# Kernel tuning notes

Measured on AMD Instinct MI355X. Metric: run time of the kernel, lower is better.

## Reference

```python
import jax, jax.numpy as jnp
import numpy as np

ALPHA, BETA, THETA = 1.0, 1.0, 10.0
WIN_SIZE = 11
SIGMA = 1.5


def _gauss_window(size, sigma, channel):
    g = np.exp(-((np.arange(size) - size // 2) ** 2) / (2.0 * sigma ** 2))
    g = g / g.sum()
    w2 = np.outer(g, g).astype(np.float32)  # [k, k]
    return jnp.asarray(np.tile(w2[None, None], (channel, 1, 1, 1)))  # [C,1,k,k]


def _dwconv_valid(x, w):
    # x: [B,C,H,W], w: [C,1,k,k]; depthwise conv, no padding (matches F.conv2d padd=0, groups=C)
    return jax.lax.conv_general_dilated(
        x, w, window_strides=(1, 1), padding='VALID',
        feature_group_count=x.shape[1],
        dimension_numbers=('NCHW', 'OIHW', 'NCHW'))


def _ssim_loss(img1, img2, window):
    # val_range heuristic: inputs in [0,1) -> L = 1
    L = 1.0
    C1 = (0.01 * L) ** 2
    C2 = (0.03 * L) ** 2
    mu1 = _dwconv_valid(img1, window)
    mu2 = _dwconv_valid(img2, window)
    mu1_sq = mu1 * mu1
    mu2_sq = mu2 * mu2
    mu1_mu2 = mu1 * mu2
    sigma1_sq = _dwconv_valid(img1 * img1, window) - mu1_sq
    sigma2_sq = _dwconv_valid(img2 * img2, window) - mu2_sq
    sigma12 = _dwconv_valid(img1 * img2, window) - mu1_mu2
    v1 = 2.0 * sigma12 + C2
    v2 = sigma1_sq + sigma2_sq + C2
    ssim_map = (2.0 * mu1_mu2 + C1) * v1 / ((mu1_sq + mu2_sq + C1) * v2)
    return 1.0 - jnp.mean(ssim_map)


_LAP2D = np.array([[1.0, 1.0, 1.0],
                   [1.0, -8.0, 1.0],
                   [1.0, 1.0, 1.0]], dtype=np.float32) / 16.0  # kornia normalized (abs-sum=16)


def _laplacian(x):
    # kornia.filters.laplacian(x, 3): reflect padding, normalized 3x3 laplacian, depthwise
    c = x.shape[1]
    k = jnp.asarray(np.tile(_LAP2D[None, None], (c, 1, 1, 1)))  # [C,1,3,3]
    xp = jnp.pad(x, ((0, 0), (0, 0), (1, 1), (1, 1)), mode='reflect')
    return _dwconv_valid(xp, k)


def setup_inputs() -> dict:
    key = jax.random.key(0)
    ks = jax.random.split(key, 5)
    shape = (32, 1, 512, 512)
    names = ['im_fus', 'im_ir', 'im_vi', 'map_ir', 'map_vi']
    return {n: jax.random.uniform(k, shape, dtype=jnp.float32) for n, k in zip(names, ks)}


def reference(im_fus, im_ir, im_vi, map_ir, map_vi):
    window = _gauss_window(WIN_SIZE, SIGMA, im_fus.shape[1])
    ms_ssim_loss = _ssim_loss(im_fus, im_ir, window) + _ssim_loss(im_fus, im_vi, window)
    l1_loss = jnp.mean(jnp.abs(jnp.maximum(map_ir, map_vi) - im_fus))
    ir_grad = jnp.abs(_laplacian(im_ir))
    vi_grad = jnp.abs(_laplacian(im_vi))
    fus_grad = jnp.abs(_laplacian(im_fus))
    grad_loss = jnp.mean(jnp.abs(jnp.maximum(ir_grad, vi_grad) - fus_grad))
    return ALPHA * ms_ssim_loss + BETA * l1_loss + THETA * grad_loss
```

## Files before the change

kernel.cpp:

```cpp
#include <hip/hip_runtime.h>
#include <cmath>


typedef float f32x2 __attribute__((ext_vector_type(2)));

struct GaussW { float w[11]; };

#define SSIM_C1 1.0e-4f
#define SSIM_C2 9.0e-4f

#define SSIM_STEP(P, RF, RG, RV, RF2, RG2, RV2)                               \
    {                                                                         \
        const int r = rb + (P);                                               \
        if (r < in_rows) {                            \
                  \
            srow_fi[wv][lane] = (f32x2){RF, RG};                              \
            srow_v [wv][lane] = RV;                                           \
            if (extra) {                                                      \
                srow_fi[wv][64 + lane] = (f32x2){RF2, RG2};                   \
                srow_v [wv][64 + lane] = RV2;                                 \
            }                                                                 \
            __builtin_amdgcn_wave_barrier();           \
                        \
            if (r + 2 < in_rows) {                                            \
                const size_t base = (size_t)(r0 + r + 2) * 512 + col;         \
                RF = Fp[base]; RG = Ip[base]; RV = Vp[base];                  \
                if (extra_ok) {                                               \
                    const size_t b2 = (size_t)(r0 + r + 2) * 512 + col2;      \
                    RF2 = Fp[b2]; RG2 = Ip[b2]; RV2 = Vp[b2];                 \
                }                                                             \
            }                                                                 \
                     \
            f32x2 hfhi  = (f32x2)(0.f);                   \
            f32x2 hffii = (f32x2)(0.f);                   \
            f32x2 hfifv = (f32x2)(0.f);                   \
            f32x2 hvvv  = (f32x2)(0.f);                   \
            _Pragma("unroll")                                                 \
            for (int k = 0; k < 11; ++k) {                                    \
                const float t = w6[k < 6 ? k : 10 - k];                       \
                const f32x2 fi = srow_fi[wv][lane + k];                       \
                const float V  = srow_v [wv][lane + k];                       \
                const f32x2 t2 = (f32x2){t, t};                               \
                const f32x2 tfi = t2 * fi;                                    \
                hfhi  = __builtin_elementwise_fma(t2,  fi, hfhi);             \
                hffii = __builtin_elementwise_fma(tfi, fi, hffii);            \
                hfifv.x = fmaf(tfi.x, fi.y, hfifv.x);                         \
                hfifv.y = fmaf(tfi.x, V,    hfifv.y);                         \
                const float tV = t * V;                                       \
                hvvv.x = fmaf(t,  V, hvvv.x);                                 \
                hvvv.y = fmaf(tV, V, hvvv.y);                                 \
            }                                                                 \
            __builtin_amdgcn_wave_barrier();            \
                        \
            {                                                                 \
                const f32x2 w02 = (f32x2){w6[0], w6[0]};                      \
                acc[(P) % 11][0] = w02 * hfhi;                                \
                acc[(P) % 11][1] = w02 * hffii;                               \
                acc[(P) % 11][2] = w02 * hfifv;                               \
                acc[(P) % 11][3] = w02 * hvvv;                                \
            }                                                                 \
            _Pragma("unroll")                                                 \
            for (int k = 1; k < 11; ++k) {                                    \
                const int s = ((P) - k + 22) % 11;                            \
                const float t = w6[k < 6 ? k : 10 - k];                       \
                const f32x2 t2 = (f32x2){t, t};                               \
                acc[s][0] = __builtin_elementwise_fma(t2, hfhi,  acc[s][0]);  \
                acc[s][1] = __builtin_elementwise_fma(t2, hffii, acc[s][1]);  \
                acc[s][2] = __builtin_elementwise_fma(t2, hfifv, acc[s][2]);  \
                acc[s][3] = __builtin_elementwise_fma(t2, hvvv,  acc[s][3]);  \
            }                                                                 \
                  \
            if (r >= 10) {                                                    \
                const int s = ((P) + 1) % 11;                                 \
                const float mu1 = acc[s][0].x, mu2 = acc[s][0].y;             \
                const float mu3 = acc[s][3].x;                                \
                const float eff = acc[s][1].x, eii = acc[s][1].y;             \
                const float evv = acc[s][3].y;                                \
                const float efi = acc[s][2].x, efv = acc[s][2].y;             \
                const float mu1sq = mu1*mu1, mu2sq = mu2*mu2, mu3sq = mu3*mu3;\
                const float mu12 = mu1*mu2, mu13 = mu1*mu3;                   \
                const float sf  = eff - mu1sq;                                \
                const float si  = eii - mu2sq;                                \
                const float sv  = evv - mu3sq;                                \
                const float s12 = efi - mu12;                                 \
                const float s13 = efv - mu13;                                 \
                const float n1 = (2.f*mu12 + SSIM_C1) * (2.f*s12 + SSIM_C2);  \
                const float d1 = (mu1sq + mu2sq + SSIM_C1) * (sf + si + SSIM_C2); \
                const float n2 = (2.f*mu13 + SSIM_C1) * (2.f*s13 + SSIM_C2);  \
                const float d2 = (mu1sq + mu3sq + SSIM_C1) * (sf + sv + SSIM_C2); \
                const float q1 = __builtin_amdgcn_rcpf(d1);                   \
                const float q2 = __builtin_amdgcn_rcpf(d2);                   \
                if (col_ok) lssim += fmaf(n1, q1, n2 * q2);                   \
            }                                                                 \
        }                                                                     \
    }

__global__ __launch_bounds__(256, 2)
void ssim_kernel(const float* __restrict__ fus, const float* __restrict__ irp,
                 const float* __restrict__ vip, float* __restrict__ part,
                 GaussW gw)
{
    const int b    = blockIdx.z;
    const int r0   = blockIdx.y * 42;
    const int tid  = threadIdx.x;
    const int wv   = tid >> 6;
    const int lane = tid & 63;
    const int c0   = blockIdx.x * 256 + wv * 64;
    const int out_rows = min(42, 502 - r0);
    const int in_rows  = out_rows + 10;

    const size_t ib = (size_t)b * 512 * 512;
    const float* __restrict__ Fp = fus + ib;
    const float* __restrict__ Ip = irp + ib;
    const float* __restrict__ Vp = vip + ib;

    __shared__ f32x2 srow_fi[4][80];
    __shared__ float srow_v [4][80];

    float w6[6];
#pragma unroll
    for (int k = 0; k < 6; ++k) w6[k] = gw.w[k];

    f32x2 acc[11][4];
#pragma unroll
    for (int s = 0; s < 11; ++s)
#pragma unroll
        for (int q = 0; q < 4; ++q) acc[s][q] = (f32x2)(0.f);

    float lssim = 0.f;
    const int  col      = c0 + lane;
    const bool col_ok   = col <= 501;
    const bool extra    = lane < 10;
    const int  col2     = c0 + 64 + lane;
    const bool extra_ok = extra && (col2 < 512);

    float arf, arg, arv, arf2 = 0.f, arg2 = 0.f, arv2 = 0.f;
    float brf, brg, brv, brf2 = 0.f, brg2 = 0.f, brv2 = 0.f;
    {
        const size_t b0 = (size_t)r0 * 512 + col;
        arf = Fp[b0]; arg = Ip[b0]; arv = Vp[b0];
        const size_t b1 = (size_t)(r0 + 1) * 512 + col;
        brf = Fp[b1]; brg = Ip[b1]; brv = Vp[b1];
        if (extra_ok) {
            const size_t c20 = (size_t)r0 * 512 + col2;
            arf2 = Fp[c20]; arg2 = Ip[c20]; arv2 = Vp[c20];
            const size_t c21 = (size_t)(r0 + 1) * 512 + col2;
            brf2 = Fp[c21]; brg2 = Ip[c21]; brv2 = Vp[c21];
        }
    }

#pragma unroll 1
    for (int rb = 0; rb < 66; rb += 22) {
        SSIM_STEP(0,  arf, arg, arv, arf2, arg2, arv2)
        SSIM_STEP(1,  brf, brg, brv, brf2, brg2, brv2)
        SSIM_STEP(2,  arf, arg, arv, arf2, arg2, arv2)
        SSIM_STEP(3,  brf, brg, brv, brf2, brg2, brv2)
        SSIM_STEP(4,  arf, arg, arv, arf2, arg2, arv2)
        SSIM_STEP(5,  brf, brg, brv, brf2, brg2, brv2)
        SSIM_STEP(6,  arf, arg, arv, arf2, arg2, arv2)
        SSIM_STEP(7,  brf, brg, brv, brf2, brg2, brv2)
        SSIM_STEP(8,  arf, arg, arv, arf2, arg2, arv2)
        SSIM_STEP(9,  brf, brg, brv, brf2, brg2, brv2)
        SSIM_STEP(10, arf, arg, arv, arf2, arg2, arv2)
        SSIM_STEP(11, brf, brg, brv, brf2, brg2, brv2)
        SSIM_STEP(12, arf, arg, arv, arf2, arg2, arv2)
        SSIM_STEP(13, brf, brg, brv, brf2, brg2, brv2)
        SSIM_STEP(14, arf, arg, arv, arf2, arg2, arv2)
        SSIM_STEP(15, brf, brg, brv, brf2, brg2, brv2)
        SSIM_STEP(16, arf, arg, arv, arf2, arg2, arv2)
        SSIM_STEP(17, brf, brg, brv, brf2, brg2, brv2)
        SSIM_STEP(18, arf, arg, arv, arf2, arg2, arv2)
        SSIM_STEP(19, brf, brg, brv, brf2, brg2, brv2)
        SSIM_STEP(20, arf, arg, arv, arf2, arg2, arv2)
        SSIM_STEP(21, brf, brg, brv, brf2, brg2, brv2)
    }

#pragma unroll
    for (int off = 32; off > 0; off >>= 1)
        lssim += __shfl_down(lssim, off);
    __shared__ float red[4];
    if (lane == 0) red[wv] = lssim;
    __syncthreads();
    if (tid == 0) {
        const int blk = blockIdx.x + 2 * (blockIdx.y + 12 * blockIdx.z);
        part[blk] = red[0] + red[1] + red[2] + red[3];
    }
}

__device__ inline float4 lap3x3(const float* __restrict__ rm,
                                const float* __restrict__ rc,
                                const float* __restrict__ rp,
                                int x0, int xl, int xr, float4& center)
{
    float4 a = *(const float4*)(rm + x0);
    float4 b = *(const float4*)(rc + x0);
    float4 c = *(const float4*)(rp + x0);
    const float aL = rm[xl], bL = rc[xl], cL = rp[xl];
    const float aR = rm[xr], bR = rc[xr], cR = rp[xr];
    const float s0 = aL + bL + cL;
    const float s1 = a.x + b.x + c.x;
    const float s2 = a.y + b.y + c.y;
    const float s3 = a.z + b.z + c.z;
    const float s4 = a.w + b.w + c.w;
    const float s5 = aR + bR + cR;
    center = b;
    float4 l;
    l.x = (s0 + s1 + s2 - 9.f*b.x) * 0.0625f;
    l.y = (s1 + s2 + s3 - 9.f*b.y) * 0.0625f;
    l.z = (s2 + s3 + s4 - 9.f*b.z) * 0.0625f;
    l.w = (s3 + s4 + s5 - 9.f*b.w) * 0.0625f;
    return l;
}

__global__ __launch_bounds__(256, 4)
void lapl1_kernel(const float* __restrict__ fus, const float* __restrict__ irp,
                  const float* __restrict__ vip, const float* __restrict__ mir,
                  const float* __restrict__ mvi,
                  float* __restrict__ part_l1, float* __restrict__ part_gr)
{
    const int b   = blockIdx.y;
    const int tid = threadIdx.x;
    const int xq  = tid & 127;
    const int x0  = xq * 4;
    const size_t ib = (size_t)b * 512 * 512;

    const int xl = (x0 == 0)        ? 1   : x0 - 1;
    const int xr = (x0 + 4 == 512)  ? 510 : x0 + 4;

    const float* Fb = fus + ib;
    const float* Ib = irp + ib;
    const float* Vb = vip + ib;

    float l1s = 0.f, grs = 0.f;

#pragma unroll
    for (int it = 0; it < 4; ++it) {
        const int y  = blockIdx.x * 8 + it * 2 + (tid >> 7);
        const int ym = (y == 0)   ? 1   : y - 1;
        const int yp = (y == 511) ? 510 : y + 1;

        float4 cf, ci, cv;
        const float4 lf = lap3x3(Fb + (size_t)ym*512, Fb + (size_t)y*512, Fb + (size_t)yp*512, x0, xl, xr, cf);
        const float4 li = lap3x3(Ib + (size_t)ym*512, Ib + (size_t)y*512, Ib + (size_t)yp*512, x0, xl, xr, ci);
        const float4 lv = lap3x3(Vb + (size_t)ym*512, Vb + (size_t)y*512, Vb + (size_t)yp*512, x0, xl, xr, cv);

        const float4 m1 = *(const float4*)(mir + ib + (size_t)y*512 + x0);
        const float4 m2 = *(const float4*)(mvi + ib + (size_t)y*512 + x0);

        l1s += fabsf(fmaxf(m1.x, m2.x) - cf.x) + fabsf(fmaxf(m1.y, m2.y) - cf.y)
             + fabsf(fmaxf(m1.z, m2.z) - cf.z) + fabsf(fmaxf(m1.w, m2.w) - cf.w);

        grs += fabsf(fmaxf(fabsf(li.x), fabsf(lv.x)) - fabsf(lf.x))
             + fabsf(fmaxf(fabsf(li.y), fabsf(lv.y)) - fabsf(lf.y))
             + fabsf(fmaxf(fabsf(li.z), fabsf(lv.z)) - fabsf(lf.z))
             + fabsf(fmaxf(fabsf(li.w), fabsf(lv.w)) - fabsf(lf.w));
    }

#pragma unroll
    for (int off = 32; off > 0; off >>= 1) {
        l1s += __shfl_down(l1s, off);
        grs += __shfl_down(grs, off);
    }
    __shared__ float red[8];
    if ((tid & 63) == 0) { red[tid >> 6] = l1s; red[4 + (tid >> 6)] = grs; }
    __syncthreads();
    if (tid == 0) {
        const int blk = blockIdx.x + 64 * blockIdx.y;
        part_l1[blk] = red[0] + red[1] + red[2] + red[3];
        part_gr[blk] = red[4] + red[5] + red[6] + red[7];
    }
}

__global__ void final_kernel(const float* __restrict__ ws, float* __restrict__ out)
{
    const int tid = threadIdx.x;
    float s0 = 0.f, s1 = 0.f, s2 = 0.f;
#pragma unroll
    for (int i = tid; i < 768; i += 256) s0 += ws[i];
#pragma unroll
    for (int i = tid; i < 2048; i += 256) {
        s1 += ws[768 + i];
        s2 += ws[2816 + i];
    }
#pragma unroll
    for (int off = 32; off > 0; off >>= 1) {
        s0 += __shfl_down(s0, off);
        s1 += __shfl_down(s1, off);
        s2 += __shfl_down(s2, off);
    }
    __shared__ float red[12];
    if ((tid & 63) == 0) {
        red[tid >> 6] = s0; red[4 + (tid >> 6)] = s1; red[8 + (tid >> 6)] = s2;
    }
    __syncthreads();
    if (tid == 0) {
        const float ssim_sum = red[0] + red[1] + red[2] + red[3];
        const float l1_sum   = red[4] + red[5] + red[6] + red[7];
        const float gr_sum   = red[8] + red[9] + red[10] + red[11];
        const float ms = 2.f - ssim_sum / 8064128.f;
        const float l1 = l1_sum / 8388608.f;
        const float gr = gr_sum / 8388608.f;
        out[0] = ms + l1 + 10.f * gr;
    }
}

extern "C" void kernel_launch(void* const* d_in, const int* in_sizes, int n_in,
                              void* d_out, int out_size, void* d_ws, size_t ws_size,
                              hipStream_t stream)
{
    const float* fus = (const float*)d_in[0];
    const float* irp = (const float*)d_in[1];
    const float* vip = (const float*)d_in[2];
    const float* mir = (const float*)d_in[3];
    const float* mvi = (const float*)d_in[4];
    float* out = (float*)d_out;
    float* ws  = (float*)d_ws;

    GaussW gw;
    double g[11], s = 0.0;
    for (int i = 0; i < 11; ++i) {
        const double d = (double)i - 5.0;
        g[i] = std::exp(-(d * d) / (2.0 * 1.5 * 1.5));
        s += g[i];
    }
    for (int i = 0; i < 11; ++i) gw.w[i] = (float)(g[i] / s);

    ssim_kernel<<<dim3(2, 12, 32), 256, 0, stream>>>(fus, irp, vip, ws, gw);
    lapl1_kernel<<<dim3(64, 32), 256, 0, stream>>>(fus, irp, vip, mir, mvi,
                                                   ws + 768, ws + 2816);
    final_kernel<<<1, 256, 0, stream>>>(ws, out);
}
```

Measured before the change: 110.8 us.

## Fuse Laplacian gradient and L1 losses into the streaming SSIM kernel

Removes the separate lapl1 kernel and computes the 3x3 Laplacian gradient loss and the L1 loss inside the SSIM row-streaming kernel. It reuses the F/I/V rows already staged in shared memory, keeping rolling column sums and handling reflect padding at image and tile borders. This avoids re-reading the three images from global memory and drops one launch, at the cost of more registers and branches in an already register-heavy unrolled loop at 2 blocks per SM.

```diff
diff --git a/kernel.cpp b/kernel.cpp
--- a/kernel.cpp
+++ b/kernel.cpp
@@ -9,19 +9,20 @@
 #define SSIM_C1 1.0e-4f
 #define SSIM_C2 9.0e-4f
 
-#define SSIM_STEP(P, RF, RG, RV, RF2, RG2, RV2)                               \
+#define SSIM_STEP(P, RF, RG, RV, RF2, RG2, RV2, RFL, RGL, RVL, RM1, RM2)      \
     {                                                                         \
         const int r = rb + (P);                                               \
         if (r < in_rows) {                            \
-                  \
+            const float curF = RF, curI = RG, curV = RV;                      \
+                                                             \
             srow_fi[wv][lane] = (f32x2){RF, RG};                              \
             srow_v [wv][lane] = RV;                                           \
-            if (extra) {                                                      \
-                srow_fi[wv][64 + lane] = (f32x2){RF2, RG2};                   \
-                srow_v [wv][64 + lane] = RV2;                                 \
-            }                                                                 \
+            if (extra)  { srow_fi[wv][64 + lane] = (f32x2){RF2, RG2};         \
+                          srow_v [wv][64 + lane] = RV2; }                     \
+            if (extraL) { srow_fi[wv][74] = (f32x2){RFL, RGL};                \
+                          srow_v [wv][74] = RVL; }                            \
             __builtin_amdgcn_wave_barrier();           \
-                        \
+             \
             if (r + 2 < in_rows) {                                            \
                 const size_t base = (size_t)(r0 + r + 2) * 512 + col;         \
                 RF = Fp[base]; RG = Ip[base]; RV = Vp[base];                  \
@@ -29,12 +30,22 @@
                     const size_t b2 = (size_t)(r0 + r + 2) * 512 + col2;      \
                     RF2 = Fp[b2]; RG2 = Ip[b2]; RV2 = Vp[b2];                 \
                 }                                                             \
+                if (extraL) {                                                 \
+                    const size_t bl = (size_t)(r0 + r + 2) * 512 + colL;      \
+                    RFL = Fp[bl]; RGL = Ip[bl]; RVL = Vp[bl];                 \
+                }                                                             \
+            }                                                                 \
+             \
+            const float um1 = RM1, um2 = RM2;                                 \
+            if (((r + 2) <= 43 || last) && (r + 2) < in_rows) {               \
+                const size_t bm = (size_t)(r0 + r + 1) * 512 + col;           \
+                RM1 = mir[bm]; RM2 = mvi[bm];                                 \
             }                                                                 \
                      \
-            f32x2 hfhi  = (f32x2)(0.f);                   \
-            f32x2 hffii = (f32x2)(0.f);                   \
-            f32x2 hfifv = (f32x2)(0.f);                   \
-            f32x2 hvvv  = (f32x2)(0.f);                   \
+            f32x2 hfhi  = (f32x2)(0.f);                                       \
+            f32x2 hffii = (f32x2)(0.f);                                       \
+            f32x2 hfifv = (f32x2)(0.f);                                       \
+            f32x2 hvvv  = (f32x2)(0.f);                                       \
             _Pragma("unroll")                                                 \
             for (int k = 0; k < 11; ++k) {                                    \
                 const float t = w6[k < 6 ? k : 10 - k];                       \
@@ -50,8 +61,18 @@
                 hvvv.x = fmaf(t,  V, hvvv.x);                                 \
                 hvvv.y = fmaf(tV, V, hvvv.y);                                 \
             }                                                                 \
+             \
+            f32x2 csFI_cur = (f32x2)(0.f); float csV_cur = 0.f;               \
+            if ((rb + (P)) <= 43 || last) {                                   \
+                const f32x2 fiL = srow_fi[wv][il];                            \
+                const f32x2 fiR = srow_fi[wv][ir_];                           \
+                const float vsL = srow_v[wv][il];                             \
+                const float vsR = srow_v[wv][ir_];                            \
+                csFI_cur = fiL + fiR + (f32x2){curF, curI};                   \
+                csV_cur  = vsL + vsR + curV;                                  \
+            }                                                                 \
             __builtin_amdgcn_wave_barrier();            \
-                        \
+               \
             {                                                                 \
                 const f32x2 w02 = (f32x2){w6[0], w6[0]};                      \
                 acc[(P) % 11][0] = w02 * hfhi;                                \
@@ -69,7 +90,7 @@
                 acc[s][2] = __builtin_elementwise_fma(t2, hfifv, acc[s][2]);  \
                 acc[s][3] = __builtin_elementwise_fma(t2, hvvv,  acc[s][3]);  \
             }                                                                 \
-                  \
+                                           \
             if (r >= 10) {                                                    \
                 const int s = ((P) + 1) % 11;                                 \
                 const float mu1 = acc[s][0].x, mu2 = acc[s][0].y;             \
@@ -92,27 +113,58 @@
                 const float q2 = __builtin_amdgcn_rcpf(d2);                   \
                 if (col_ok) lssim += fmaf(n1, q1, n2 * q2);                   \
             }                                                                 \
+             \
+            if (r >= 2 && ((rb + (P)) <= 43 || last)) {                       \
+                const f32x2 sFI = csFI_2 + csFI_1 + csFI_cur;                 \
+                const float sV  = csV_2 + csV_1 + csV_cur;                    \
+                const f32x2 lFI = __builtin_elementwise_fma(                  \
+                                     (f32x2){-9.f,-9.f}, cPrevFI, sFI);       \
+                const float lV  = fmaf(-9.f, cPrevV, sV);                     \
+                grs += fabsf(fmaxf(fabsf(lFI.y), fabsf(lV)) - fabsf(lFI.x));  \
+                l1s += fabsf(fmaxf(um1, um2) - cPrevFI.x);                    \
+            }                                                                 \
+            if (first && (rb + (P)) == 1) {   \
+                const f32x2 sFI = csFI_1 + csFI_cur + csFI_cur;               \
+                const float sV  = csV_1 + csV_cur + csV_cur;                  \
+                const f32x2 lFI = __builtin_elementwise_fma(                  \
+                                     (f32x2){-9.f,-9.f}, cPrevFI, sFI);       \
+                const float lV  = fmaf(-9.f, cPrevV, sV);                     \
+                grs += fabsf(fmaxf(fabsf(lFI.y), fabsf(lV)) - fabsf(lFI.x));  \
+                l1s += fabsf(fmaxf(um1, um2) - cPrevFI.x);                    \
+            }                                                                 \
+                                             \
+            if ((rb + (P)) <= 43 || last) {                                   \
+                csFI_2 = csFI_1; csFI_1 = csFI_cur;                           \
+                csV_2  = csV_1;  csV_1  = csV_cur;                            \
+                cPrevFI = (f32x2){curF, curI}; cPrevV = curV;                 \
+            }                                                                 \
         }                                                                     \
     }
 
 __global__ __launch_bounds__(256, 2)
 void ssim_kernel(const float* __restrict__ fus, const float* __restrict__ irp,
-                 const float* __restrict__ vip, float* __restrict__ part,
+                 const float* __restrict__ vip, const float* __restrict__ mir,
+                 const float* __restrict__ mvi, float* __restrict__ ws,
                  GaussW gw)
 {
     const int b    = blockIdx.z;
-    const int r0   = blockIdx.y * 42;
+    const int rs   = blockIdx.y;
+    const int r0   = rs * 42;
     const int tid  = threadIdx.x;
     const int wv   = tid >> 6;
     const int lane = tid & 63;
     const int c0   = blockIdx.x * 256 + wv * 64;
     const int out_rows = min(42, 502 - r0);
     const int in_rows  = out_rows + 10;
+    const bool first = (rs == 0);
+    const bool last  = (rs == 11);
 
     const size_t ib = (size_t)b * 512 * 512;
     const float* __restrict__ Fp = fus + ib;
     const float* __restrict__ Ip = irp + ib;
     const float* __restrict__ Vp = vip + ib;
+    mir += ib;
+    mvi += ib;
 
     __shared__ f32x2 srow_fi[4][80];
     __shared__ float srow_v [4][80];
@@ -127,15 +179,26 @@
 #pragma unroll
         for (int q = 0; q < 4; ++q) acc[s][q] = (f32x2)(0.f);
 
-    float lssim = 0.f;
+    float lssim = 0.f, l1s = 0.f, grs = 0.f;
     const int  col      = c0 + lane;
     const bool col_ok   = col <= 501;
     const bool extra    = lane < 10;
     const int  col2     = c0 + 64 + lane;
     const bool extra_ok = extra && (col2 < 512);
+    const bool extraL   = (lane == 10) && (c0 > 0);
+    const int  colL     = c0 - 1;
+    const int il  = (lane == 0)  ? ((c0 == 0) ? 1 : 74) : (lane - 1);
+    const int ir_ = (lane == 63) ? ((c0 + 64 >= 512) ? 62 : 64) : (lane + 1);
+
+    f32x2 csFI_1 = (f32x2)(0.f), csFI_2 = (f32x2)(0.f);
+    float csV_1 = 0.f, csV_2 = 0.f;
+    f32x2 cPrevFI = (f32x2)(0.f); float cPrevV = 0.f;
 
     float arf, arg, arv, arf2 = 0.f, arg2 = 0.f, arv2 = 0.f;
     float brf, brg, brv, brf2 = 0.f, brg2 = 0.f, brv2 = 0.f;
+    float aRFL = 0.f, aRGL = 0.f, aRVL = 0.f;
+    float bRFL = 0.f, bRGL = 0.f, bRVL = 0.f;
+    float mA1 = 0.f, mA2 = 0.f, mB1, mB2;
     {
         const size_t b0 = (size_t)r0 * 512 + col;
         arf = Fp[b0]; arg = Ip[b0]; arv = Vp[b0];
@@ -147,127 +210,67 @@
             const size_t c21 = (size_t)(r0 + 1) * 512 + col2;
             brf2 = Fp[c21]; brg2 = Ip[c21]; brv2 = Vp[c21];
         }
+        if (extraL) {
+            const size_t l0 = (size_t)r0 * 512 + colL;
+            aRFL = Fp[l0]; aRGL = Ip[l0]; aRVL = Vp[l0];
+            const size_t l1x = (size_t)(r0 + 1) * 512 + colL;
+            bRFL = Fp[l1x]; bRGL = Ip[l1x]; bRVL = Vp[l1x];
+        }
+        const size_t bm = (size_t)r0 * 512 + col;
+        mB1 = mir[bm]; mB2 = mvi[bm];
     }
 
 #pragma unroll 1
     for (int rb = 0; rb < 66; rb += 22) {
-        SSIM_STEP(0,  arf, arg, arv, arf2, arg2, arv2)
-        SSIM_STEP(1,  brf, brg, brv, brf2, brg2, brv2)
-        SSIM_STEP(2,  arf, arg, arv, arf2, arg2, arv2)
-        SSIM_STEP(3,  brf, brg, brv, brf2, brg2, brv2)
-        SSIM_STEP(4,  arf, arg, arv, arf2, arg2, arv2)
-        SSIM_STEP(5,  brf, brg, brv, brf2, brg2, brv2)
-        SSIM_STEP(6,  arf, arg, arv, arf2, arg2, arv2)
-        SSIM_STEP(7,  brf, brg, brv, brf2, brg2, brv2)
-        SSIM_STEP(8,  arf, arg, arv, arf2, arg2, arv2)
-        SSIM_STEP(9,  brf, brg, brv, brf2, brg2, brv2)
-        SSIM_STEP(10, arf, arg, arv, arf2, arg2, arv2)
-        SSIM_STEP(11, brf, brg, brv, brf2, brg2, brv2)
-        SSIM_STEP(12, arf, arg, arv, arf2, arg2, arv2)
-        SSIM_STEP(13, brf, brg, brv, brf2, brg2, brv2)
-        SSIM_STEP(14, arf, arg, arv, arf2, arg2, arv2)
-        SSIM_STEP(15, brf, brg, brv, brf2, brg2, brv2)
-        SSIM_STEP(16, arf, arg, arv, arf2, arg2, arv2)
-        SSIM_STEP(17, brf, brg, brv, brf2, brg2, brv2)
-        SSIM_STEP(18, arf, arg, arv, arf2, arg2, arv2)
-        SSIM_STEP(19, brf, brg, brv, brf2, brg2, brv2)
-        SSIM_STEP(20, arf, arg, arv, arf2, arg2, arv2)
-        SSIM_STEP(21, brf, brg, brv, brf2, brg2, brv2)
-    }
-
-#pragma unroll
-    for (int off = 32; off > 0; off >>= 1)
+        SSIM_STEP(0,  arf, arg, arv, arf2, arg2, arv2, aRFL, aRGL, aRVL, mA1, mA2)
+        SSIM_STEP(1,  brf, brg, brv, brf2, brg2, brv2, bRFL, bRGL, bRVL, mB1, mB2)
+        SSIM_STEP(2,  arf, arg, arv, arf2, arg2, arv2, aRFL, aRGL, aRVL, mA1, mA2)
+        SSIM_STEP(3,  brf, brg, brv, brf2, brg2, brv2, bRFL, bRGL, bRVL, mB1, mB2)
+        SSIM_STEP(4,  arf, arg, arv, arf2, arg2, arv2, aRFL, aRGL, aRVL, mA1, mA2)
+        SSIM_STEP(5,  brf, brg, brv, brf2, brg2, brv2, bRFL, bRGL, bRVL, mB1, mB2)
+        SSIM_STEP(6,  arf, arg, arv, arf2, arg2, arv2, aRFL, aRGL, aRVL, mA1, mA2)
+        SSIM_STEP(7,  brf, brg, brv, brf2, brg2, brv2, bRFL, bRGL, bRVL, mB1, mB2)
+        SSIM_STEP(8,  arf, arg, arv, arf2, arg2, arv2, aRFL, aRGL, aRVL, mA1, mA2)
+        SSIM_STEP(9,  brf, brg, brv, brf2, brg2, brv2, bRFL, bRGL, bRVL, mB1, mB2)
+        SSIM_STEP(10, arf, arg, arv, arf2, arg2, arv2, aRFL, aRGL, aRVL, mA1, mA2)
+        SSIM_STEP(11, brf, brg, brv, brf2, brg2, brv2, bRFL, bRGL, bRVL, mB1, mB2)
+        SSIM_STEP(12, arf, arg, arv, arf2, arg2, arv2, aRFL, aRGL, aRVL, mA1, mA2)
+        SSIM_STEP(13, brf, brg, brv, brf2, brg2, brv2, bRFL, bRGL, bRVL, mB1, mB2)
+        SSIM_STEP(14, arf, arg, arv, arf2, arg2, arv2, aRFL, aRGL, aRVL, mA1, mA2)
+        SSIM_STEP(15, brf, brg, brv, brf2, brg2, brv2, bRFL, bRGL, bRVL, mB1, mB2)
+        SSIM_STEP(16, arf, arg, arv, arf2, arg2, arv2, aRFL, aRGL, aRVL, mA1, mA2)
+        SSIM_STEP(17, brf, brg, brv, brf2, brg2, brv2, bRFL, bRGL, bRVL, mB1, mB2)
+        SSIM_STEP(18, arf, arg, arv, arf2, arg2, arv2, aRFL, aRGL, aRVL, mA1, mA2)
+        SSIM_STEP(19, brf, brg, brv, brf2, brg2, brv2, bRFL, bRGL, bRVL, mB1, mB2)
+        SSIM_STEP(20, arf, arg, arv, arf2, arg2, arv2, aRFL, aRGL, aRVL, mA1, mA2)
+        SSIM_STEP(21, brf, brg, brv, brf2, brg2, brv2, bRFL, bRGL, bRVL, mB1, mB2)
+    }
+
+    if (last) {
+        const size_t bm = (size_t)511 * 512 + col;
+        const float m1e = mir[bm], m2e = mvi[bm];
+        const f32x2 sFI = csFI_2 + csFI_2 + csFI_1;
+        const float sV  = csV_2 + csV_2 + csV_1;
+        const f32x2 lFI = __builtin_elementwise_fma((f32x2){-9.f,-9.f}, cPrevFI, sFI);
+        const float lV  = fmaf(-9.f, cPrevV, sV);
+        grs += fabsf(fmaxf(fabsf(lFI.y), fabsf(lV)) - fabsf(lFI.x));
+        l1s += fabsf(fmaxf(m1e, m2e) - cPrevFI.x);
+    }
+
+#pragma unroll
+    for (int off = 32; off > 0; off >>= 1) {
         lssim += __shfl_down(lssim, off);
-    __shared__ float red[4];
-    if (lane == 0) red[wv] = lssim;
+        l1s   += __shfl_down(l1s, off);
+        grs   += __shfl_down(grs, off);
+    }
+    __shared__ float red[12];
+    if (lane == 0) { red[wv] = lssim; red[4 + wv] = l1s; red[8 + wv] = grs; }
     __syncthreads();
     if (tid == 0) {
         const int blk = blockIdx.x + 2 * (blockIdx.y + 12 * blockIdx.z);
-        part[blk] = red[0] + red[1] + red[2] + red[3];
-    }
-}
-
-__device__ inline float4 lap3x3(const float* __restrict__ rm,
-                                const float* __restrict__ rc,
-                                const float* __restrict__ rp,
-                                int x0, int xl, int xr, float4& center)
-{
-    float4 a = *(const float4*)(rm + x0);
-    float4 b = *(const float4*)(rc + x0);
-    float4 c = *(const float4*)(rp + x0);
-    const float aL = rm[xl], bL = rc[xl], cL = rp[xl];
-    const float aR = rm[xr], bR = rc[xr], cR = rp[xr];
-    const float s0 = aL + bL + cL;
-    const float s1 = a.x + b.x + c.x;
-    const float s2 = a.y + b.y + c.y;
-    const float s3 = a.z + b.z + c.z;
-    const float s4 = a.w + b.w + c.w;
-    const float s5 = aR + bR + cR;
-    center = b;
-    float4 l;
-    l.x = (s0 + s1 + s2 - 9.f*b.x) * 0.0625f;
-    l.y = (s1 + s2 + s3 - 9.f*b.y) * 0.0625f;
-    l.z = (s2 + s3 + s4 - 9.f*b.z) * 0.0625f;
-    l.w = (s3 + s4 + s5 - 9.f*b.w) * 0.0625f;
-    return l;
-}
-
-__global__ __launch_bounds__(256, 4)
-void lapl1_kernel(const float* __restrict__ fus, const float* __restrict__ irp,
-                  const float* __restrict__ vip, const float* __restrict__ mir,
-                  const float* __restrict__ mvi,
-                  float* __restrict__ part_l1, float* __restrict__ part_gr)
-{
-    const int b   = blockIdx.y;
-    const int tid = threadIdx.x;
-    const int xq  = tid & 127;
-    const int x0  = xq * 4;
-    const size_t ib = (size_t)b * 512 * 512;
-
-    const int xl = (x0 == 0)        ? 1   : x0 - 1;
-    const int xr = (x0 + 4 == 512)  ? 510 : x0 + 4;
-
-    const float* Fb = fus + ib;
-    const float* Ib = irp + ib;
-    const float* Vb = vip + ib;
-
-    float l1s = 0.f, grs = 0.f;
-
-#pragma unroll
-    for (int it = 0; it < 4; ++it) {
-        const int y  = blockIdx.x * 8 + it * 2 + (tid >> 7);
-        const int ym = (y == 0)   ? 1   : y - 1;
-        const int yp = (y == 511) ? 510 : y + 1;
-
-        float4 cf, ci, cv;
-        const float4 lf = lap3x3(Fb + (size_t)ym*512, Fb + (size_t)y*512, Fb + (size_t)yp*512, x0, xl, xr, cf);
-        const float4 li = lap3x3(Ib + (size_t)ym*512, Ib + (size_t)y*512, Ib + (size_t)yp*512, x0, xl, xr, ci);
-        const float4 lv = lap3x3(Vb + (size_t)ym*512, Vb + (size_t)y*512, Vb + (size_t)yp*512, x0, xl, xr, cv);
-
-        const float4 m1 = *(const float4*)(mir + ib + (size_t)y*512 + x0);
-        const float4 m2 = *(const float4*)(mvi + ib + (size_t)y*512 + x0);
-
-        l1s += fabsf(fmaxf(m1.x, m2.x) - cf.x) + fabsf(fmaxf(m1.y, m2.y) - cf.y)
-             + fabsf(fmaxf(m1.z, m2.z) - cf.z) + fabsf(fmaxf(m1.w, m2.w) - cf.w);
-
-        grs += fabsf(fmaxf(fabsf(li.x), fabsf(lv.x)) - fabsf(lf.x))
-             + fabsf(fmaxf(fabsf(li.y), fabsf(lv.y)) - fabsf(lf.y))
-             + fabsf(fmaxf(fabsf(li.z), fabsf(lv.z)) - fabsf(lf.z))
-             + fabsf(fmaxf(fabsf(li.w), fabsf(lv.w)) - fabsf(lf.w));
-    }
-
-#pragma unroll
-    for (int off = 32; off > 0; off >>= 1) {
-        l1s += __shfl_down(l1s, off);
-        grs += __shfl_down(grs, off);
-    }
-    __shared__ float red[8];
-    if ((tid & 63) == 0) { red[tid >> 6] = l1s; red[4 + (tid >> 6)] = grs; }
-    __syncthreads();
-    if (tid == 0) {
-        const int blk = blockIdx.x + 64 * blockIdx.y;
-        part_l1[blk] = red[0] + red[1] + red[2] + red[3];
-        part_gr[blk] = red[4] + red[5] + red[6] + red[7];
+        ws[blk]        = red[0] + red[1] + red[2] + red[3];
+        ws[768 + blk]  = red[4] + red[5] + red[6] + red[7];
+        ws[1536 + blk] = (red[8] + red[9] + red[10] + red[11]) * 0.0625f;
     }
 }
 
@@ -276,11 +279,10 @@
     const int tid = threadIdx.x;
     float s0 = 0.f, s1 = 0.f, s2 = 0.f;
 #pragma unroll
-    for (int i = tid; i < 768; i += 256) s0 += ws[i];
-#pragma unroll
-    for (int i = tid; i < 2048; i += 256) {
+    for (int i = tid; i < 768; i += 256) {
+        s0 += ws[i];
         s1 += ws[768 + i];
-        s2 += ws[2816 + i];
+        s2 += ws[1536 + i];
     }
 #pragma unroll
     for (int off = 32; off > 0; off >>= 1) {
@@ -325,8 +327,7 @@
     }
     for (int i = 0; i < 11; ++i) gw.w[i] = (float)(g[i] / s);
 
-    ssim_kernel<<<dim3(2, 12, 32), 256, 0, stream>>>(fus, irp, vip, ws, gw);
-    lapl1_kernel<<<dim3(64, 32), 256, 0, stream>>>(fus, irp, vip, mir, mvi,
-                                                   ws + 768, ws + 2816);
+    ssim_kernel<<<dim3(2, 12, 32), 256, 0, stream>>>(fus, irp, vip, mir, mvi,
+                                                     ws, gw);
     final_kernel<<<1, 256, 0, stream>>>(ws, out);
 }
```

New measurement: 103.8 us. -6.3%, faster.
